# Performance work log

Hardware: AMD Instinct MI355X
Metric: run time of the kernel (lower is better)

## Reference

```python
import jax, jax.numpy as jnp
import numpy as np

LATENT_DIM = 16
ORDER = 4


def _build_indices(d, order):
    """Replicates Moment.__init__ exactly, but reduced to index pairs.

    At iteration z the original builds a [n_z, d] 0/1 matrix M with
    M[k, i] = 1 iff k >= offsets[i], where offsets[i] = n_z - S[i] and
    S[i] = number of flattened id-list elements in groups i..d-1
    (group sizes update as suffix sums each iteration). The call then
    computes prev[..., k] * x[..., j] at positions where M[k, j] == 1,
    flattened row-major (k major, j minor) -- identical to np.nonzero order.
    """
    c = np.ones(d, dtype=np.int64)
    pairs = []
    for _ in range(order - 1):
        S = np.cumsum(c[::-1])[::-1]          # S[i] = sum_{j>=i} c[j]
        n = int(S[0])                          # rows of the (transposed) matrix
        offsets = n - S                        # left-padding per column
        keep = np.arange(n)[:, None] >= offsets[None, :]   # [n, d] mask == (M > 0)
        k_idx, j_idx = np.nonzero(keep)        # row-major: matches reshape([n*d]) + boolean_mask
        pairs.append((jnp.asarray(k_idx), jnp.asarray(j_idx)))
        c = S
    return pairs


_PAIRS = _build_indices(LATENT_DIM, ORDER)


def setup_inputs() -> dict:
    key = jax.random.key(0)
    inputs = jax.random.normal(key, (4, 2048, LATENT_DIM), dtype=jnp.float32)
    return {"inputs": inputs}


def reference(inputs):
    # inputs: [B, T, d]
    feats = [inputs]
    for k_idx, j_idx in _PAIRS:
        prev = feats[-1]                                   # [B, T, n_z]
        # Direct gather of the unique (as selected by the original masks)
        # outer-product terms: prev[..., k] * x[..., j] where mask is 1.
        feats.append(jnp.take(prev, k_idx, axis=-1) * jnp.take(inputs, j_idx, axis=-1))
    ones = jnp.ones(inputs.shape[:2] + (1,), dtype=inputs.dtype)   # order-0 moment
    return jnp.concatenate([ones] + feats, axis=-1)        # [B, T, C(d+order, order)]
```

## Files before the change

kernel.cpp:

```cpp
#include <hip/hip_runtime.h>
#include <stdint.h>


#define D    16
#define NC   4845
#define N2   136
#define N4   3876
#define LDSZ 153

struct Tables {
    unsigned short chan[NC];
    unsigned short p2pair[N2];
};

static constexpr int slot2(int a, int b) { return a * (a + 1) / 2 + b; }

static constexpr Tables build_tables() {
    Tables t{};
    long c[D] = {};
    for (int i = 0; i < D; ++i) c[i] = 1;
    int tupPrev[N4][4] = {};
    int tupNext[N4][4] = {};
    for (int i = 0; i < D; ++i) {
        tupPrev[i][0] = i; tupPrev[i][1] = 16; tupPrev[i][2] = 16; tupPrev[i][3] = 16;
    }
    int pos = 0;
    t.chan[pos++] = (unsigned short)(16 | (16 << 8));
    for (int i = 0; i < D; ++i) t.chan[pos++] = (unsigned short)(i | (16 << 8));
    for (int it = 0; it < 3; ++it) {
        long S[D] = {};
        long acc = 0;
        for (int i = D - 1; i >= 0; --i) { acc += c[i]; S[i] = acc; }
        const long n = S[0];
        long off[D] = {};
        for (int i = 0; i < D; ++i) off[i] = n - S[i];
        const int len = it + 2;
        int cnt = 0;
        for (long k = 0; k < n; ++k) {
            for (int j = 0; j < D; ++j) {
                if (k >= off[j]) {
                    int nt[4];
                    for (int q = 0; q < 4; ++q) nt[q] = tupPrev[k][q];
                    nt[len - 1] = j;
                    for (int q = 0; q < 4; ++q) tupNext[cnt][q] = nt[q];
                    ++cnt;
                    int s[4] = {16, 16, 16, 16};
                    for (int q = 0; q < len; ++q) s[q] = nt[q];
                    for (int a = 1; a < len; ++a) {
                        int v = s[a]; int b = a - 1;
                        while (b >= 0 && s[b] < v) { s[b + 1] = s[b]; --b; }
                        s[b + 1] = v;
                    }
                    unsigned e;
                    if (len == 2)      e = (unsigned)s[0] | ((unsigned)s[1] << 8);
                    else if (len == 3) e = (unsigned)(17 + slot2(s[0], s[1])) | ((unsigned)s[2] << 8);
                    else               e = (unsigned)(17 + slot2(s[0], s[1]))
                                         | ((unsigned)(17 + slot2(s[2], s[3])) << 8);
                    t.chan[pos++] = (unsigned short)e;
                }
            }
        }
        for (int i = 0; i < D; ++i) c[i] = S[i];
        for (int i = 0; i < cnt; ++i)
            for (int q = 0; q < 4; ++q) tupPrev[i][q] = tupNext[i][q];
    }
    int m = 0;
    for (int k = 0; k < D; ++k)
        for (int j = 0; j <= k; ++j)
            t.p2pair[m++] = (unsigned short)(k | (j << 8));
    return t;
}

__device__ const Tables d_tables = build_tables();

__global__ __launch_bounds__(256) void moment_kernel(const float* __restrict__ in,
                                                     float* __restrict__ out,
                                                     int npos) {
    __shared__ float lds[LDSZ];
    const int pos = blockIdx.x;
    if (pos >= npos) return;
    const int tid = threadIdx.x;

    const float* __restrict__ xrow = in + (size_t)pos * D;
    if (tid < D) lds[tid] = xrow[tid];
    if (tid == D) lds[D] = 1.0f;
    __syncthreads();

    if (tid < N2) {
        const unsigned pk = d_tables.p2pair[tid];
        lds[17 + tid] = lds[pk & 0xFFu] * lds[pk >> 8];
    }
    __syncthreads();

    float* __restrict__ orow = out + (size_t)pos * NC;
    for (int c = tid; c < NC; c += 256) {
        const unsigned e = d_tables.chan[c];
        orow[c] = lds[e & 0xFFu] * lds[e >> 8];
    }
}

extern "C" void kernel_launch(void* const* d_in, const int* in_sizes, int n_in,
                              void* d_out, int out_size, void* d_ws, size_t ws_size,
                              hipStream_t stream) {
    const float* in = (const float*)d_in[0];
    float* out = (float*)d_out;
    const int npos = in_sizes[0] / D;
    moment_kernel<<<npos, 256, 0, stream>>>(in, out, npos);
}
```

Measured before the change: 163.8 us.

## Process four positions per block with float4 stores via flattened index table

Each block now handles four consecutive positions, so its output span is a multiple of 16 bytes and every thread can write a float4. A precomputed table of 32-bit LDS index pairs covering all four positions drives the gathers. The goal is wider, aligned global stores and fewer blocks. The cost is a table that is eight times larger (about 77 KB read per block instead of under 10 KB). The kernel also assumes npos is divisible by four and drops the bounds check.

```diff
diff --git a/kernel.cpp b/kernel.cpp
--- a/kernel.cpp
+++ b/kernel.cpp
@@ -2,21 +2,24 @@
 #include <stdint.h>
 
 
-#define D    16
-#define NC   4845
-#define N2   136
-#define N4   3876
-#define LDSZ 153
+#define D      16
+#define NC     4845
+#define N2     136
+#define N4     3876
+#define POSPB  4
+#define FLATPB (NC * POSPB)
+#define STRIDE 153
 
 struct Tables {
-    unsigned short chan[NC];
-    unsigned short p2pair[N2];
+    uint32_t chunk[FLATPB];
+    uint16_t p2pair[N2];
 };
 
 static constexpr int slot2(int a, int b) { return a * (a + 1) / 2 + b; }
 
 static constexpr Tables build_tables() {
     Tables t{};
+    unsigned short chan[NC] = {};
     long c[D] = {};
     for (int i = 0; i < D; ++i) c[i] = 1;
     int tupPrev[N4][4] = {};
@@ -25,8 +28,9 @@
         tupPrev[i][0] = i; tupPrev[i][1] = 16; tupPrev[i][2] = 16; tupPrev[i][3] = 16;
     }
     int pos = 0;
-    t.chan[pos++] = (unsigned short)(16 | (16 << 8));
-    for (int i = 0; i < D; ++i) t.chan[pos++] = (unsigned short)(i | (16 << 8));
+    chan[pos++] = (unsigned short)(16 | (16 << 8));
+    for (int i = 0; i < D; ++i)
+        chan[pos++] = (unsigned short)(i | (16 << 8));
     for (int it = 0; it < 3; ++it) {
         long S[D] = {};
         long acc = 0;
@@ -56,13 +60,20 @@
                     else if (len == 3) e = (unsigned)(17 + slot2(s[0], s[1])) | ((unsigned)s[2] << 8);
                     else               e = (unsigned)(17 + slot2(s[0], s[1]))
                                          | ((unsigned)(17 + slot2(s[2], s[3])) << 8);
-                    t.chan[pos++] = (unsigned short)e;
+                    chan[pos++] = (unsigned short)e;
                 }
             }
         }
         for (int i = 0; i < D; ++i) c[i] = S[i];
         for (int i = 0; i < cnt; ++i)
             for (int q = 0; q < 4; ++q) tupPrev[i][q] = tupNext[i][q];
+    }
+    for (int f = 0; f < FLATPB; ++f) {
+        int p = f / NC;
+        int ch = f - p * NC;
+        unsigned lo = chan[ch] & 0xFFu;
+        unsigned hi = chan[ch] >> 8;
+        t.chunk[f] = (uint32_t)(p * STRIDE + lo) | ((uint32_t)(p * STRIDE + hi) << 16);
     }
     int m = 0;
     for (int k = 0; k < D; ++k)
@@ -74,28 +85,43 @@
 __device__ const Tables d_tables = build_tables();
 
 __global__ __launch_bounds__(256) void moment_kernel(const float* __restrict__ in,
-                                                     float* __restrict__ out,
-                                                     int npos) {
-    __shared__ float lds[LDSZ];
-    const int pos = blockIdx.x;
-    if (pos >= npos) return;
+                                                     float* __restrict__ out) {
+    __shared__ float vals[POSPB * STRIDE];
     const int tid = threadIdx.x;
+    const int blk = blockIdx.x;
 
-    const float* __restrict__ xrow = in + (size_t)pos * D;
-    if (tid < D) lds[tid] = xrow[tid];
-    if (tid == D) lds[D] = 1.0f;
+    if (tid < 16) {
+        float4 v = reinterpret_cast<const float4*>(in + (size_t)blk * (POSPB * D))[tid];
+        const int p  = tid >> 2;
+        const int i0 = (tid & 3) * 4;
+        vals[p * STRIDE + i0 + 0] = v.x;
+        vals[p * STRIDE + i0 + 1] = v.y;
+        vals[p * STRIDE + i0 + 2] = v.z;
+        vals[p * STRIDE + i0 + 3] = v.w;
+    } else if (tid < 16 + POSPB) {
+        vals[(tid - 16) * STRIDE + 16] = 1.0f;
+    }
     __syncthreads();
 
     if (tid < N2) {
         const unsigned pk = d_tables.p2pair[tid];
-        lds[17 + tid] = lds[pk & 0xFFu] * lds[pk >> 8];
+        const unsigned a = pk & 0xFFu, b = pk >> 8;
+        #pragma unroll
+        for (int p = 0; p < POSPB; ++p)
+            vals[p * STRIDE + 17 + tid] = vals[p * STRIDE + a] * vals[p * STRIDE + b];
     }
     __syncthreads();
 
-    float* __restrict__ orow = out + (size_t)pos * NC;
-    for (int c = tid; c < NC; c += 256) {
-        const unsigned e = d_tables.chan[c];
-        orow[c] = lds[e & 0xFFu] * lds[e >> 8];
+    float4* __restrict__ ochunk = reinterpret_cast<float4*>(out + (size_t)blk * FLATPB);
+    const uint4* __restrict__ tab = reinterpret_cast<const uint4*>(d_tables.chunk);
+    for (int q = tid; q < NC; q += 256) {
+        const uint4 e = tab[q];
+        float4 v;
+        v.x = vals[e.x & 0xFFFFu] * vals[e.x >> 16];
+        v.y = vals[e.y & 0xFFFFu] * vals[e.y >> 16];
+        v.z = vals[e.z & 0xFFFFu] * vals[e.z >> 16];
+        v.w = vals[e.w & 0xFFFFu] * vals[e.w >> 16];
+        ochunk[q] = v;
     }
 }
 
@@ -105,5 +131,6 @@
     const float* in = (const float*)d_in[0];
     float* out = (float*)d_out;
     const int npos = in_sizes[0] / D;
-    moment_kernel<<<npos, 256, 0, stream>>>(in, out, npos);
+    const int nblk = npos / POSPB;
+    moment_kernel<<<nblk, 256, 0, stream>>>(in, out);
 }
```

Result: no change. 161.1 us (-1.7%).

## Process four positions per block with float4 nontemporal stores and staged LDS products

Applied to the files above, without the earlier changes.

Each block now handles four consecutive positions, so the output chunk is contiguous and can be written with 16-byte nontemporal vector stores instead of scalar stores. Intermediate order-2 and order-3 products are computed once per position in shared memory, and a precomputed per-chunk index table gives the two LDS operands for every output element. The goal is to cut launch and block overhead and raise store efficiency on this write-bound kernel. The cost is a larger constexpr table that has to be read, and the launch now assumes npos is divisible by four.

```diff
diff --git a/kernel.cpp b/kernel.cpp
--- a/kernel.cpp
+++ b/kernel.cpp
@@ -2,31 +2,29 @@
 #include <stdint.h>
 
 
-#define D    16
-#define NC   4845
-#define N2   136
-#define N4   3876
-#define LDSZ 153
+#define D      16
+#define NC     4845
+#define NPAD   4864
+#define POSPB  4
+#define STRIDE 969
+
+typedef float    f4_t __attribute__((ext_vector_type(4)));
+typedef uint32_t u4_t __attribute__((ext_vector_type(4)));
 
 struct Tables {
-    unsigned short chan[NC];
-    unsigned short p2pair[N2];
+    uint32_t chunk[NPAD * 4];
 };
-
-static constexpr int slot2(int a, int b) { return a * (a + 1) / 2 + b; }
 
 static constexpr Tables build_tables() {
     Tables t{};
+    unsigned short A[NC] = {}, B[NC] = {};
+    int pos = 0;
+    A[pos] = 0; B[pos] = 0; ++pos;
+    for (int i = 0; i < D; ++i) { A[pos] = 0; B[pos] = (unsigned short)(1 + i); ++pos; }
     long c[D] = {};
     for (int i = 0; i < D; ++i) c[i] = 1;
-    int tupPrev[N4][4] = {};
-    int tupNext[N4][4] = {};
-    for (int i = 0; i < D; ++i) {
-        tupPrev[i][0] = i; tupPrev[i][1] = 16; tupPrev[i][2] = 16; tupPrev[i][3] = 16;
-    }
-    int pos = 0;
-    t.chan[pos++] = (unsigned short)(16 | (16 << 8));
-    for (int i = 0; i < D; ++i) t.chan[pos++] = (unsigned short)(i | (16 << 8));
+    int baseprev = 1;
+    const int basecur[3] = {17, 153, 969};
     for (int it = 0; it < 3; ++it) {
         long S[D] = {};
         long acc = 0;
@@ -34,68 +32,73 @@
         const long n = S[0];
         long off[D] = {};
         for (int i = 0; i < D; ++i) off[i] = n - S[i];
-        const int len = it + 2;
-        int cnt = 0;
-        for (long k = 0; k < n; ++k) {
-            for (int j = 0; j < D; ++j) {
+        for (long k = 0; k < n; ++k)
+            for (int j = 0; j < D; ++j)
                 if (k >= off[j]) {
-                    int nt[4];
-                    for (int q = 0; q < 4; ++q) nt[q] = tupPrev[k][q];
-                    nt[len - 1] = j;
-                    for (int q = 0; q < 4; ++q) tupNext[cnt][q] = nt[q];
-                    ++cnt;
-                    int s[4] = {16, 16, 16, 16};
-                    for (int q = 0; q < len; ++q) s[q] = nt[q];
-                    for (int a = 1; a < len; ++a) {
-                        int v = s[a]; int b = a - 1;
-                        while (b >= 0 && s[b] < v) { s[b + 1] = s[b]; --b; }
-                        s[b + 1] = v;
-                    }
-                    unsigned e;
-                    if (len == 2)      e = (unsigned)s[0] | ((unsigned)s[1] << 8);
-                    else if (len == 3) e = (unsigned)(17 + slot2(s[0], s[1])) | ((unsigned)s[2] << 8);
-                    else               e = (unsigned)(17 + slot2(s[0], s[1]))
-                                         | ((unsigned)(17 + slot2(s[2], s[3])) << 8);
-                    t.chan[pos++] = (unsigned short)e;
+                    A[pos] = (unsigned short)(baseprev + (int)k);
+                    B[pos] = (unsigned short)(1 + j);
+                    ++pos;
                 }
-            }
-        }
+        baseprev = basecur[it];
         for (int i = 0; i < D; ++i) c[i] = S[i];
-        for (int i = 0; i < cnt; ++i)
-            for (int q = 0; q < 4; ++q) tupPrev[i][q] = tupNext[i][q];
     }
-    int m = 0;
-    for (int k = 0; k < D; ++k)
-        for (int j = 0; j <= k; ++j)
-            t.p2pair[m++] = (unsigned short)(k | (j << 8));
+    for (int f = 0; f < NPAD * 4; ++f) {
+        const int p = f / NC;
+        const int ch = f - p * NC;
+        if (p < POSPB)
+            t.chunk[f] = (uint32_t)(p * STRIDE + A[ch])
+                       | ((uint32_t)(p * STRIDE + B[ch]) << 16);
+        else
+            t.chunk[f] = 0;
+    }
     return t;
 }
 
 __device__ const Tables d_tables = build_tables();
 
 __global__ __launch_bounds__(256) void moment_kernel(const float* __restrict__ in,
-                                                     float* __restrict__ out,
-                                                     int npos) {
-    __shared__ float lds[LDSZ];
-    const int pos = blockIdx.x;
-    if (pos >= npos) return;
+                                                     float* __restrict__ out) {
+    __shared__ float lds[POSPB * STRIDE];
     const int tid = threadIdx.x;
+    const int blk = blockIdx.x;
+    const uint32_t* __restrict__ dtab = d_tables.chunk;
 
-    const float* __restrict__ xrow = in + (size_t)pos * D;
-    if (tid < D) lds[tid] = xrow[tid];
-    if (tid == D) lds[D] = 1.0f;
-    __syncthreads();
-
-    if (tid < N2) {
-        const unsigned pk = d_tables.p2pair[tid];
-        lds[17 + tid] = lds[pk & 0xFFu] * lds[pk >> 8];
+    if (tid < 64) {
+        const float v = in[(size_t)blk * (POSPB * D) + tid];
+        lds[(tid >> 4) * STRIDE + 1 + (tid & 15)] = v;
+    } else if (tid < 68) {
+        lds[(tid - 64) * STRIDE] = 1.0f;
     }
     __syncthreads();
 
-    float* __restrict__ orow = out + (size_t)pos * NC;
-    for (int c = tid; c < NC; c += 256) {
-        const unsigned e = d_tables.chan[c];
-        orow[c] = lds[e & 0xFFu] * lds[e >> 8];
+    for (int i = tid; i < 136 * POSPB; i += 256) {
+        const int ch = 17 + (i >> 2);
+        const int po = (i & 3) * STRIDE;
+        const uint32_t e = dtab[ch];
+        lds[po + ch] = lds[po + (e & 0xFFFFu)] * lds[po + (e >> 16)];
+    }
+    __syncthreads();
+
+    for (int i = tid; i < 816 * POSPB; i += 256) {
+        const int ch = 153 + (i >> 2);
+        const int po = (i & 3) * STRIDE;
+        const uint32_t e = dtab[ch];
+        lds[po + ch] = lds[po + (e & 0xFFFFu)] * lds[po + (e >> 16)];
+    }
+    __syncthreads();
+
+    f4_t* __restrict__ ochunk = (f4_t*)(out + (size_t)blk * (NC * POSPB));
+    const u4_t* __restrict__ tab4 = (const u4_t*)dtab;
+    #pragma unroll 4
+    for (int it2 = 0; it2 < 19; ++it2) {
+        const int q = tid + it2 * 256;
+        const u4_t e = tab4[q];
+        f4_t v;
+        v.x = lds[e.x & 0xFFFFu] * lds[e.x >> 16];
+        v.y = lds[e.y & 0xFFFFu] * lds[e.y >> 16];
+        v.z = lds[e.z & 0xFFFFu] * lds[e.z >> 16];
+        v.w = lds[e.w & 0xFFFFu] * lds[e.w >> 16];
+        if (q < NC) __builtin_nontemporal_store(v, &ochunk[q]);
     }
 }
 
@@ -105,5 +108,6 @@
     const float* in = (const float*)d_in[0];
     float* out = (float*)d_out;
     const int npos = in_sizes[0] / D;
-    moment_kernel<<<npos, 256, 0, stream>>>(in, out, npos);
+    const int nblk = npos / POSPB;
+    moment_kernel<<<nblk, 256, 0, stream>>>(in, out);
 }
```

Measured after the change: 180.5 us. +10.1%, slower.
